# Performance work log

Measured on AMD Instinct MI355X. Metric: run time of the kernel, lower is better.

## Reference

```python
import jax, jax.numpy as jnp
import numpy as np

B, D, N_CLASSES = 8192, 128, 512
MARGIN, GAMMA = 0.25, 256.0
NEG_INF = -1e9  # effectively -inf; logits are O(gamma*2) ~ 512 in magnitude


def setup_inputs() -> dict:
    key = jax.random.key(0)
    k1, k2 = jax.random.split(key)
    feat = jax.random.normal(k1, (B, D), dtype=jnp.float32)
    label = jax.random.randint(k2, (B,), 0, N_CLASSES, dtype=jnp.int64)
    return {"feat": feat, "label": label}


def reference(feat, label):
    m, gamma = MARGIN, GAMMA
    O_p, O_n = 1.0 + m, -m
    delta_p, delta_n = 1.0 - m, m

    # L2-normalize rows (eps clamp as in F.normalize)
    norm = jnp.maximum(jnp.linalg.norm(feat, axis=1, keepdims=True), 1e-12)
    f = feat / norm
    sim = f @ f.T  # [B, B]

    same = label[:, None] == label[None, :]
    eye = jnp.eye(sim.shape[0], dtype=bool)
    pos_mask = same & ~eye
    neg_mask = ~same

    sim_d = jax.lax.stop_gradient(sim)  # .detach() in torch
    alpha_p = jax.nn.relu(O_p - sim_d)
    alpha_n = jax.nn.relu(sim_d - O_n)

    logit_p = -gamma * alpha_p * (sim - delta_p)
    logit_n = gamma * alpha_n * (sim - delta_n)

    # Per-row masked logsumexp over positives / negatives
    lse_p = jax.nn.logsumexp(jnp.where(pos_mask, logit_p, NEG_INF), axis=1)
    lse_n = jax.nn.logsumexp(jnp.where(neg_mask, logit_n, NEG_INF), axis=1)

    # Rows with no positives or no negatives are skipped in the original loop
    valid = pos_mask.any(axis=1) & neg_mask.any(axis=1)
    loss_i = jax.nn.softplus(lse_n + lse_p)
    n_valid = jnp.maximum(valid.sum(), 1)
    return jnp.sum(jnp.where(valid, loss_i, 0.0)) / n_valid
```

## Files before the change

kernel.cpp:

```cpp
#include <hip/hip_runtime.h>
#include <hip/hip_bf16.h>

typedef short bf16x8 __attribute__((ext_vector_type(8)));
typedef float f32x4 __attribute__((ext_vector_type(4)));

#define B_ROWS 8192
#define DIM 128
#define NCLS 512
#define MMAX 64
#define NSLICE 64
#define NPAIR 2080

#define G2 369.32993f
#define G2D16B 87.083121f
#define LN2F 0.69314718056f

__global__ __launch_bounds__(256) void prep_k(const float* __restrict__ feat,
                                              unsigned int* __restrict__ fbp,
                                              int* __restrict__ ctrl) {
    const int T = blockIdx.x;
    const int t = threadIdx.x;
    if (T == 0 && t < 4) ctrl[t] = 0;
    const int rr = t >> 4, q = t & 15;
    const int row = T * 16 + rr;
    const float4* f4 = (const float4*)(feat + row * DIM + q * 8);
    const float4 v0 = f4[0], v1 = f4[1];
    float ss = v0.x * v0.x + v0.y * v0.y + v0.z * v0.z + v0.w * v0.w
             + v1.x * v1.x + v1.y * v1.y + v1.z * v1.z + v1.w * v1.w;
    #pragma unroll
    for (int d = 1; d < 16; d <<= 1) ss += __shfl_xor(ss, d);
    const float inv = 1.0f / fmaxf(sqrtf(ss), 1e-12f);
    const float e[8] = {v0.x, v0.y, v0.z, v0.w, v1.x, v1.y, v1.z, v1.w};
    unsigned int w[4];
    #pragma unroll
    for (int j = 0; j < 4; ++j) {
        __hip_bfloat16 lo = __float2bfloat16(e[2 * j] * inv);
        __hip_bfloat16 hi = __float2bfloat16(e[2 * j + 1] * inv);
        w[j] = (unsigned int)*(unsigned short*)&lo |
               ((unsigned int)*(unsigned short*)&hi << 16);
    }
    const int g = (T * 4 + (q >> 2)) * 256 + (q & 3) * 64 + rr * 4;
    *(uint4*)(fbp + g) = make_uint4(w[0], w[1], w[2], w[3]);
}

#define ELEM(sv) __builtin_amdgcn_exp2f(fminf(fmaf(fmaxf((sv), -0.25f) * fmaxf((sv), -0.25f), G2, -G2D16B), 56.f))

__global__ __launch_bounds__(256, 4) void mega_k(const unsigned short* __restrict__ fb_,
                                                 const int* __restrict__ label,
                                                 float* __restrict__ PR,
                                                 float* __restrict__ lse2_p,
                                                 float* __restrict__ lse2_same) {
    __shared__ float colS[4][128];
    __shared__ unsigned int F[MMAX][MMAX + 1];
    __shared__ int rlw[4][MMAX];
    __shared__ int rl[MMAX];
    __shared__ int cntw[4];

    const int bid = blockIdx.x;
    const int tid = threadIdx.x;
    const int wv = tid >> 6, ln = tid & 63;

    if (bid < NPAIR) {
        int I = (int)((129.0f - sqrtf(16641.0f - 8.0f * (float)bid)) * 0.5f);
        while (I * 64 - I * (I - 1) / 2 > bid) --I;
        while ((I + 1) * 64 - (I + 1) * I / 2 <= bid) ++I;
        const int J = I + (bid - (I * 64 - I * (I - 1) / 2));
        const bool offd = (I != J);

        const int lc = ln & 15, lg = ln >> 4;
        const int wv2 = wv * 2;
        const bf16x8* pk = (const bf16x8*)fb_;

        const int Ta0 = I * 8 + wv2;
        bf16x8 a0[4], a1[4];
        #pragma unroll
        for (int k = 0; k < 4; ++k) {
            a0[k] = pk[(Ta0 * 4 + k) * 64 + ln];
            a1[k] = pk[((Ta0 + 1) * 4 + k) * 64 + ln];
        }

        float Sr0 = 0.f, Sr1 = 0.f;
        bf16x8 bA[4], bB[4];
        const bf16x8* pB = pk + J * 2048 + ln;

        #define LOADB(dst, base) { \
            _Pragma("unroll") \
            for (int k = 0; k < 4; ++k) dst[k] = (base)[k * 64]; }

        #define STEP(bR, t) { \
            f32x4 acc0 = {0.f, 0.f, 0.f, 0.f}, acc1 = acc0; \
            _Pragma("unroll") \
            for (int k = 0; k < 4; ++k) { \
                acc0 = __builtin_amdgcn_mfma_f32_16x16x32_bf16(bR[k], a0[k], acc0, 0, 0, 0); \
                acc1 = __builtin_amdgcn_mfma_f32_16x16x32_bf16(bR[k], a1[k], acc1, 0, 0, 0); \
            } \
            float e00 = ELEM(acc0[0]), e01 = ELEM(acc0[1]); \
            float e02 = ELEM(acc0[2]), e03 = ELEM(acc0[3]); \
            float e10 = ELEM(acc1[0]), e11 = ELEM(acc1[1]); \
            float e12 = ELEM(acc1[2]), e13 = ELEM(acc1[3]); \
            if (!offd && (t) == wv2) { \
                const int base = lg * 4; \
                e00 = (base + 0 == lc) ? 0.f : e00; \
                e01 = (base + 1 == lc) ? 0.f : e01; \
                e02 = (base + 2 == lc) ? 0.f : e02; \
                e03 = (base + 3 == lc) ? 0.f : e03; \
            } \
            if (!offd && (t) == wv2 + 1) { \
                const int base = lg * 4; \
                e10 = (base + 0 == lc) ? 0.f : e10; \
                e11 = (base + 1 == lc) ? 0.f : e11; \
                e12 = (base + 2 == lc) ? 0.f : e12; \
                e13 = (base + 3 == lc) ? 0.f : e13; \
            } \
            Sr0 += (e00 + e01) + (e02 + e03); \
            Sr1 += (e10 + e11) + (e12 + e13); \
            if (offd) { \
                float c0 = e00 + e10, c1 = e01 + e11; \
                float c2 = e02 + e12, c3 = e03 + e13; \
                _Pragma("unroll") \
                for (int d = 1; d < 16; d <<= 1) { \
                    c0 += __shfl_xor(c0, d); c1 += __shfl_xor(c1, d); \
                    c2 += __shfl_xor(c2, d); c3 += __shfl_xor(c3, d); \
                } \
                if (lc == 0) \
                    *(float4*)&colS[wv][(t) * 16 + lg * 4] = make_float4(c0, c1, c2, c3); \
            } }

        LOADB(bA, pB);
        #pragma unroll 1
        for (int t = 0; t < 8; t += 2) {
            LOADB(bB, pB + 256);
            STEP(bA, t);
            if (t + 2 < 8) LOADB(bA, pB + 512);
            STEP(bB, t + 1);
            pB += 512;
        }
        #undef LOADB
        #undef STEP

        #pragma unroll
        for (int d = 16; d < 64; d <<= 1) {
            Sr0 += __shfl_xor(Sr0, d);
            Sr1 += __shfl_xor(Sr1, d);
        }
        if (lg == 0) {
            const int r = I * 128 + wv * 32 + lc;
            PR[J * B_ROWS + r]      = Sr0;
            PR[J * B_ROWS + r + 16] = Sr1;
        }

        if (offd) {
            __syncthreads();
            if (tid < 128) {
                const float tot = colS[0][tid] + colS[1][tid] +
                                  colS[2][tid] + colS[3][tid];
                PR[I * B_ROWS + J * 128 + tid] = tot;
            }
        }
        return;
    }

    const int c = bid - NPAIR;
    {
        int cnt = 0;
        #pragma unroll 1
        for (int it = 0; it < 8; ++it) {
            const int4 L = ((const int4*)label)[wv * 512 + it * 64 + ln];
            const int lv[4] = {L.x, L.y, L.z, L.w};
            #pragma unroll
            for (int j = 0; j < 4; ++j) {
                const bool hit = (lv[j] == c);
                const unsigned long long mask = __ballot(hit);
                const int below = __popcll(mask & ((1ull << ln) - 1ull));
                const int slot = cnt + below;
                if (hit && slot < MMAX) rlw[wv][slot] = wv * 2048 + it * 256 + ln * 4 + j;
                cnt += __popcll(mask);
            }
        }
        if (ln == 0) cntw[wv] = cnt;
    }
    __syncthreads();
    const int c0 = cntw[0], c1 = cntw[1], c2 = cntw[2], c3 = cntw[3];
    const int total = c0 + c1 + c2 + c3;
    const int m = total < MMAX ? total : MMAX;
    if (m == 0) return;
    const bool row_valid = (total >= 2) && (total < B_ROWS);
    {
        const int offs = (wv > 0 ? c0 : 0) + (wv > 1 ? c1 : 0) + (wv > 2 ? c2 : 0);
        const int mycnt = cntw[wv] < MMAX ? cntw[wv] : MMAX;
        if (ln < mycnt) {
            const int slot = offs + ln;
            if (slot < m) rl[slot] = rlw[wv][ln];
        }
    }
    __syncthreads();

    const unsigned int* fbp = (const unsigned int*)fb_;
    for (int i = wv; i < m; i += 4) {
        const int r = rl[i];
        const int g = ((r >> 4) * 4 + (ln >> 4)) * 256 + ((ln >> 2) & 3) * 64 +
                      (r & 15) * 4 + (ln & 3);
        F[i][ln] = fbp[g];
    }
    __syncthreads();

    for (int i = wv; i < m; i += 4) {
        float s = 0.f;
        if (ln < m) {
            #pragma unroll 8
            for (int k = 0; k < 64; ++k) {
                const unsigned int wi = F[i][k], wj = F[ln][k];
                const float li = __uint_as_float(wi << 16);
                const float hi = __uint_as_float(wi & 0xffff0000u);
                const float lj = __uint_as_float(wj << 16);
                const float hj = __uint_as_float(wj & 0xffff0000u);
                s = fmaf(li, lj, s);
                s = fmaf(hi, hj, s);
            }
        }
        const bool act = (ln < m) && (ln != i);
        const float up = 1.25f - s;
        const float lp = act ? G2 * fmaxf(up, 0.f) * (up - 0.5f) : -1e30f;
        const float un = s + 0.25f;
        const float lnn = act ? G2 * fmaxf(un, 0.f) * (un - 0.5f) : -1e30f;
        float Mp = lp, Mn = lnn;
        #pragma unroll
        for (int d = 1; d < 64; d <<= 1) {
            Mp = fmaxf(Mp, __shfl_xor(Mp, d));
            Mn = fmaxf(Mn, __shfl_xor(Mn, d));
        }
        float Sp = act ? __builtin_amdgcn_exp2f(lp - Mp) : 0.f;
        float Sn = act ? __builtin_amdgcn_exp2f(lnn - Mn) : 0.f;
        #pragma unroll
        for (int d = 1; d < 64; d <<= 1) { Sp += __shfl_xor(Sp, d); Sn += __shfl_xor(Sn, d); }
        if (ln == 0) {
            const int row = rl[i];
            lse2_p[row]    = row_valid ? (Mp + __builtin_amdgcn_logf(Sp)) : -1e30f;
            lse2_same[row] = row_valid ? (Mn + __builtin_amdgcn_logf(Sn)) : -1e30f;
        }
    }
}

__global__ __launch_bounds__(256) void finalize_k(const float* __restrict__ PR,
                                                  const float* __restrict__ lse2_p,
                                                  const float* __restrict__ lse2_same,
                                                  int* __restrict__ ctrl,
                                                  float* __restrict__ out) {
    const int r = blockIdx.x * 256 + threadIdx.x;
    float local = 0.f; int c = 0;
    const float lp2 = lse2_p[r];
    if (lp2 > -1e29f) {
        float pa = 0.f, pb = 0.f, pc = 0.f, pd = 0.f;
        #pragma unroll
        for (int s = 0; s < NSLICE; s += 4) {
            pa += PR[(s + 0) * B_ROWS + r];
            pb += PR[(s + 1) * B_ROWS + r];
            pc += PR[(s + 2) * B_ROWS + r];
            pd += PR[(s + 3) * B_ROWS + r];
        }
        const float Sa = (pa + pb) + (pc + pd);
        const float lse2_all = __builtin_amdgcn_logf(Sa) + 64.f;
        const float d = lse2_same[r] - lse2_all;
        const float corr = __builtin_amdgcn_logf(fmaxf(1.f - __builtin_amdgcn_exp2f(d), 1e-30f));
        const float z = LN2F * (lp2 + lse2_all + corr);
        local = fmaxf(z, 0.f) + log1pf(expf(-fabsf(z)));
        c = 1;
    }
    #pragma unroll
    for (int d = 1; d < 64; d <<= 1) { local += __shfl_xor(local, d); c += __shfl_xor(c, d); }
    __shared__ float wsum[4];
    __shared__ int wcnt[4];
    const int wv = threadIdx.x >> 6;
    if ((threadIdx.x & 63) == 0) { wsum[wv] = local; wcnt[wv] = c; }
    __syncthreads();
    if (threadIdx.x == 0) {
        const float ts = wsum[0] + wsum[1] + wsum[2] + wsum[3];
        const int tc = wcnt[0] + wcnt[1] + wcnt[2] + wcnt[3];
        atomicAdd((float*)&ctrl[1], ts);
        atomicAdd(&ctrl[2], tc);
        __threadfence();
        const int ticket = atomicAdd(&ctrl[0], 1);
        if (ticket == (int)gridDim.x - 1) {
            const float gs = atomicAdd((float*)&ctrl[1], 0.0f);
            const int gc = atomicAdd(&ctrl[2], 0);
            out[0] = gs / (float)(gc > 1 ? gc : 1);
        }
    }
}

extern "C" void kernel_launch(void* const* d_in, const int* in_sizes, int n_in,
                              void* d_out, int out_size, void* d_ws, size_t ws_size,
                              hipStream_t stream) {
    const float* feat = (const float*)d_in[0];
    const int* label = (const int*)d_in[1];
    float* out = (float*)d_out;
    char* ws = (char*)d_ws;

    unsigned int* fbp = (unsigned int*)(ws);
    float* PR         = (float*)(ws + (2u << 20));
    float* lse2_p     = (float*)(ws + (4u << 20));
    float* lse2_same  = (float*)(ws + (4u << 20) + 32768);
    int*   ctrl       = (int*)  (ws + (4u << 20) + 65536);

    prep_k<<<NCLS, 256, 0, stream>>>(feat, fbp, ctrl);
    mega_k<<<NPAIR + NCLS, 256, 0, stream>>>((const unsigned short*)fbp, label,
                                             PR, lse2_p, lse2_same);
    finalize_k<<<B_ROWS / 256, 256, 0, stream>>>(PR, lse2_p, lse2_same, ctrl, out);
}
```

Before: 99.71 us.

## Move per-class positive LSE blocks from mega kernel into prep kernel

The per-class block that computes the positive and same-class log-sum-exp moves out of the MFMA pair kernel and into the prep kernel. There it runs alongside the normalization blocks and reads raw fp32 features, normalizing each row itself instead of loading the bf16 packed copy. The aim is to keep the long-tail class blocks from sharing the grid with the tiled MFMA pair blocks, and to shorten the mega kernel. The trade-off is a prep kernel that mixes heterogeneous work, larger shared memory use, and fp32 dot products that cost more per element.

```diff
diff --git a/kernel.cpp b/kernel.cpp
--- a/kernel.cpp
+++ b/kernel.cpp
@@ -16,151 +16,46 @@
 #define LN2F 0.69314718056f
 
 __global__ __launch_bounds__(256) void prep_k(const float* __restrict__ feat,
+                                              const int* __restrict__ label,
                                               unsigned int* __restrict__ fbp,
+                                              float* __restrict__ lse2_p,
+                                              float* __restrict__ lse2_same,
                                               int* __restrict__ ctrl) {
-    const int T = blockIdx.x;
-    const int t = threadIdx.x;
-    if (T == 0 && t < 4) ctrl[t] = 0;
-    const int rr = t >> 4, q = t & 15;
-    const int row = T * 16 + rr;
-    const float4* f4 = (const float4*)(feat + row * DIM + q * 8);
-    const float4 v0 = f4[0], v1 = f4[1];
-    float ss = v0.x * v0.x + v0.y * v0.y + v0.z * v0.z + v0.w * v0.w
-             + v1.x * v1.x + v1.y * v1.y + v1.z * v1.z + v1.w * v1.w;
-    #pragma unroll
-    for (int d = 1; d < 16; d <<= 1) ss += __shfl_xor(ss, d);
-    const float inv = 1.0f / fmaxf(sqrtf(ss), 1e-12f);
-    const float e[8] = {v0.x, v0.y, v0.z, v0.w, v1.x, v1.y, v1.z, v1.w};
-    unsigned int w[4];
-    #pragma unroll
-    for (int j = 0; j < 4; ++j) {
-        __hip_bfloat16 lo = __float2bfloat16(e[2 * j] * inv);
-        __hip_bfloat16 hi = __float2bfloat16(e[2 * j + 1] * inv);
-        w[j] = (unsigned int)*(unsigned short*)&lo |
-               ((unsigned int)*(unsigned short*)&hi << 16);
-    }
-    const int g = (T * 4 + (q >> 2)) * 256 + (q & 3) * 64 + rr * 4;
-    *(uint4*)(fbp + g) = make_uint4(w[0], w[1], w[2], w[3]);
-}
-
-#define ELEM(sv) __builtin_amdgcn_exp2f(fminf(fmaf(fmaxf((sv), -0.25f) * fmaxf((sv), -0.25f), G2, -G2D16B), 56.f))
-
-__global__ __launch_bounds__(256, 4) void mega_k(const unsigned short* __restrict__ fb_,
-                                                 const int* __restrict__ label,
-                                                 float* __restrict__ PR,
-                                                 float* __restrict__ lse2_p,
-                                                 float* __restrict__ lse2_same) {
-    __shared__ float colS[4][128];
-    __shared__ unsigned int F[MMAX][MMAX + 1];
+    const int bid = blockIdx.x;
+    const int tid = threadIdx.x;
+
+    if (bid < 512) {
+        if (bid == 0 && tid < 4) ctrl[tid] = 0;
+        const int T = bid;
+        const int rr = tid >> 4, q = tid & 15;
+        const int row = T * 16 + rr;
+        const float4* f4 = (const float4*)(feat + row * DIM + q * 8);
+        const float4 v0 = f4[0], v1 = f4[1];
+        float ss = v0.x * v0.x + v0.y * v0.y + v0.z * v0.z + v0.w * v0.w
+                 + v1.x * v1.x + v1.y * v1.y + v1.z * v1.z + v1.w * v1.w;
+        #pragma unroll
+        for (int d = 1; d < 16; d <<= 1) ss += __shfl_xor(ss, d);
+        const float inv = 1.0f / fmaxf(sqrtf(ss), 1e-12f);
+        const float e[8] = {v0.x, v0.y, v0.z, v0.w, v1.x, v1.y, v1.z, v1.w};
+        unsigned int w[4];
+        #pragma unroll
+        for (int j = 0; j < 4; ++j) {
+            __hip_bfloat16 lo = __float2bfloat16(e[2 * j] * inv);
+            __hip_bfloat16 hi = __float2bfloat16(e[2 * j + 1] * inv);
+            w[j] = (unsigned int)*(unsigned short*)&lo |
+                   ((unsigned int)*(unsigned short*)&hi << 16);
+        }
+        const int g = (T * 4 + (q >> 2)) * 256 + (q & 3) * 64 + rr * 4;
+        *(uint4*)(fbp + g) = make_uint4(w[0], w[1], w[2], w[3]);
+        return;
+    }
+
+    const int c = bid - 512;
+    const int wv = tid >> 6, ln = tid & 63;
+    __shared__ float F[MMAX][DIM + 1];
     __shared__ int rlw[4][MMAX];
     __shared__ int rl[MMAX];
     __shared__ int cntw[4];
-
-    const int bid = blockIdx.x;
-    const int tid = threadIdx.x;
-    const int wv = tid >> 6, ln = tid & 63;
-
-    if (bid < NPAIR) {
-        int I = (int)((129.0f - sqrtf(16641.0f - 8.0f * (float)bid)) * 0.5f);
-        while (I * 64 - I * (I - 1) / 2 > bid) --I;
-        while ((I + 1) * 64 - (I + 1) * I / 2 <= bid) ++I;
-        const int J = I + (bid - (I * 64 - I * (I - 1) / 2));
-        const bool offd = (I != J);
-
-        const int lc = ln & 15, lg = ln >> 4;
-        const int wv2 = wv * 2;
-        const bf16x8* pk = (const bf16x8*)fb_;
-
-        const int Ta0 = I * 8 + wv2;
-        bf16x8 a0[4], a1[4];
-        #pragma unroll
-        for (int k = 0; k < 4; ++k) {
-            a0[k] = pk[(Ta0 * 4 + k) * 64 + ln];
-            a1[k] = pk[((Ta0 + 1) * 4 + k) * 64 + ln];
-        }
-
-        float Sr0 = 0.f, Sr1 = 0.f;
-        bf16x8 bA[4], bB[4];
-        const bf16x8* pB = pk + J * 2048 + ln;
-
-        #define LOADB(dst, base) { \
-            _Pragma("unroll") \
-            for (int k = 0; k < 4; ++k) dst[k] = (base)[k * 64]; }
-
-        #define STEP(bR, t) { \
-            f32x4 acc0 = {0.f, 0.f, 0.f, 0.f}, acc1 = acc0; \
-            _Pragma("unroll") \
-            for (int k = 0; k < 4; ++k) { \
-                acc0 = __builtin_amdgcn_mfma_f32_16x16x32_bf16(bR[k], a0[k], acc0, 0, 0, 0); \
-                acc1 = __builtin_amdgcn_mfma_f32_16x16x32_bf16(bR[k], a1[k], acc1, 0, 0, 0); \
-            } \
-            float e00 = ELEM(acc0[0]), e01 = ELEM(acc0[1]); \
-            float e02 = ELEM(acc0[2]), e03 = ELEM(acc0[3]); \
-            float e10 = ELEM(acc1[0]), e11 = ELEM(acc1[1]); \
-            float e12 = ELEM(acc1[2]), e13 = ELEM(acc1[3]); \
-            if (!offd && (t) == wv2) { \
-                const int base = lg * 4; \
-                e00 = (base + 0 == lc) ? 0.f : e00; \
-                e01 = (base + 1 == lc) ? 0.f : e01; \
-                e02 = (base + 2 == lc) ? 0.f : e02; \
-                e03 = (base + 3 == lc) ? 0.f : e03; \
-            } \
-            if (!offd && (t) == wv2 + 1) { \
-                const int base = lg * 4; \
-                e10 = (base + 0 == lc) ? 0.f : e10; \
-                e11 = (base + 1 == lc) ? 0.f : e11; \
-                e12 = (base + 2 == lc) ? 0.f : e12; \
-                e13 = (base + 3 == lc) ? 0.f : e13; \
-            } \
-            Sr0 += (e00 + e01) + (e02 + e03); \
-            Sr1 += (e10 + e11) + (e12 + e13); \
-            if (offd) { \
-                float c0 = e00 + e10, c1 = e01 + e11; \
-                float c2 = e02 + e12, c3 = e03 + e13; \
-                _Pragma("unroll") \
-                for (int d = 1; d < 16; d <<= 1) { \
-                    c0 += __shfl_xor(c0, d); c1 += __shfl_xor(c1, d); \
-                    c2 += __shfl_xor(c2, d); c3 += __shfl_xor(c3, d); \
-                } \
-                if (lc == 0) \
-                    *(float4*)&colS[wv][(t) * 16 + lg * 4] = make_float4(c0, c1, c2, c3); \
-            } }
-
-        LOADB(bA, pB);
-        #pragma unroll 1
-        for (int t = 0; t < 8; t += 2) {
-            LOADB(bB, pB + 256);
-            STEP(bA, t);
-            if (t + 2 < 8) LOADB(bA, pB + 512);
-            STEP(bB, t + 1);
-            pB += 512;
-        }
-        #undef LOADB
-        #undef STEP
-
-        #pragma unroll
-        for (int d = 16; d < 64; d <<= 1) {
-            Sr0 += __shfl_xor(Sr0, d);
-            Sr1 += __shfl_xor(Sr1, d);
-        }
-        if (lg == 0) {
-            const int r = I * 128 + wv * 32 + lc;
-            PR[J * B_ROWS + r]      = Sr0;
-            PR[J * B_ROWS + r + 16] = Sr1;
-        }
-
-        if (offd) {
-            __syncthreads();
-            if (tid < 128) {
-                const float tot = colS[0][tid] + colS[1][tid] +
-                                  colS[2][tid] + colS[3][tid];
-                PR[I * B_ROWS + J * 128 + tid] = tot;
-            }
-        }
-        return;
-    }
-
-    const int c = bid - NPAIR;
     {
         int cnt = 0;
         #pragma unroll 1
@@ -195,12 +90,15 @@
     }
     __syncthreads();
 
-    const unsigned int* fbp = (const unsigned int*)fb_;
     for (int i = wv; i < m; i += 4) {
         const int r = rl[i];
-        const int g = ((r >> 4) * 4 + (ln >> 4)) * 256 + ((ln >> 2) & 3) * 64 +
-                      (r & 15) * 4 + (ln & 3);
-        F[i][ln] = fbp[g];
+        const float2 v = ((const float2*)feat)[r * 64 + ln];
+        float ss = v.x * v.x + v.y * v.y;
+        #pragma unroll
+        for (int d = 1; d < 64; d <<= 1) ss += __shfl_xor(ss, d);
+        const float inv = 1.0f / fmaxf(sqrtf(ss), 1e-12f);
+        F[i][2 * ln] = v.x * inv;
+        F[i][2 * ln + 1] = v.y * inv;
     }
     __syncthreads();
 
@@ -208,15 +106,7 @@
         float s = 0.f;
         if (ln < m) {
             #pragma unroll 8
-            for (int k = 0; k < 64; ++k) {
-                const unsigned int wi = F[i][k], wj = F[ln][k];
-                const float li = __uint_as_float(wi << 16);
-                const float hi = __uint_as_float(wi & 0xffff0000u);
-                const float lj = __uint_as_float(wj << 16);
-                const float hj = __uint_as_float(wj & 0xffff0000u);
-                s = fmaf(li, lj, s);
-                s = fmaf(hi, hj, s);
-            }
+            for (int k = 0; k < DIM; ++k) s = fmaf(F[i][k], F[ln][k], s);
         }
         const bool act = (ln < m) && (ln != i);
         const float up = 1.25f - s;
@@ -237,6 +127,113 @@
             const int row = rl[i];
             lse2_p[row]    = row_valid ? (Mp + __builtin_amdgcn_logf(Sp)) : -1e30f;
             lse2_same[row] = row_valid ? (Mn + __builtin_amdgcn_logf(Sn)) : -1e30f;
+        }
+    }
+}
+
+#define ELEM(sv) __builtin_amdgcn_exp2f(fminf(fmaf(fmaxf((sv), -0.25f) * fmaxf((sv), -0.25f), G2, -G2D16B), 56.f))
+
+__global__ __launch_bounds__(256, 4) void mega_k(const unsigned short* __restrict__ fb_,
+                                                 float* __restrict__ PR) {
+    __shared__ float colS[4][128];
+    const int bid = blockIdx.x;
+    const int tid = threadIdx.x;
+    const int wv = tid >> 6, ln = tid & 63;
+
+    int I = (int)((129.0f - sqrtf(16641.0f - 8.0f * (float)bid)) * 0.5f);
+    while (I * 64 - I * (I - 1) / 2 > bid) --I;
+    while ((I + 1) * 64 - (I + 1) * I / 2 <= bid) ++I;
+    const int J = I + (bid - (I * 64 - I * (I - 1) / 2));
+    const bool offd = (I != J);
+
+    const int lc = ln & 15, lg = ln >> 4;
+    const int wv2 = wv * 2;
+    const bf16x8* pk = (const bf16x8*)fb_;
+
+    const int Ta0 = I * 8 + wv2;
+    bf16x8 a0[4], a1[4];
+    #pragma unroll
+    for (int k = 0; k < 4; ++k) {
+        a0[k] = pk[(Ta0 * 4 + k) * 64 + ln];
+        a1[k] = pk[((Ta0 + 1) * 4 + k) * 64 + ln];
+    }
+
+    float Sr0 = 0.f, Sr1 = 0.f;
+    bf16x8 bA[4], bB[4];
+    const bf16x8* pB = pk + J * 2048 + ln;
+
+    #define LOADB(dst, base) { \
+        _Pragma("unroll") \
+        for (int k = 0; k < 4; ++k) dst[k] = (base)[k * 64]; }
+
+    #define STEP(bR, t) { \
+        f32x4 acc0 = {0.f, 0.f, 0.f, 0.f}, acc1 = acc0; \
+        _Pragma("unroll") \
+        for (int k = 0; k < 4; ++k) { \
+            acc0 = __builtin_amdgcn_mfma_f32_16x16x32_bf16(bR[k], a0[k], acc0, 0, 0, 0); \
+            acc1 = __builtin_amdgcn_mfma_f32_16x16x32_bf16(bR[k], a1[k], acc1, 0, 0, 0); \
+        } \
+        float e00 = ELEM(acc0[0]), e01 = ELEM(acc0[1]); \
+        float e02 = ELEM(acc0[2]), e03 = ELEM(acc0[3]); \
+        float e10 = ELEM(acc1[0]), e11 = ELEM(acc1[1]); \
+        float e12 = ELEM(acc1[2]), e13 = ELEM(acc1[3]); \
+        if (!offd && (t) == wv2) { \
+            const int base = lg * 4; \
+            e00 = (base + 0 == lc) ? 0.f : e00; \
+            e01 = (base + 1 == lc) ? 0.f : e01; \
+            e02 = (base + 2 == lc) ? 0.f : e02; \
+            e03 = (base + 3 == lc) ? 0.f : e03; \
+        } \
+        if (!offd && (t) == wv2 + 1) { \
+            const int base = lg * 4; \
+            e10 = (base + 0 == lc) ? 0.f : e10; \
+            e11 = (base + 1 == lc) ? 0.f : e11; \
+            e12 = (base + 2 == lc) ? 0.f : e12; \
+            e13 = (base + 3 == lc) ? 0.f : e13; \
+        } \
+        Sr0 += (e00 + e01) + (e02 + e03); \
+        Sr1 += (e10 + e11) + (e12 + e13); \
+        if (offd) { \
+            float c0 = e00 + e10, c1 = e01 + e11; \
+            float c2 = e02 + e12, c3 = e03 + e13; \
+            _Pragma("unroll") \
+            for (int d = 1; d < 16; d <<= 1) { \
+                c0 += __shfl_xor(c0, d); c1 += __shfl_xor(c1, d); \
+                c2 += __shfl_xor(c2, d); c3 += __shfl_xor(c3, d); \
+            } \
+            if (lc == 0) \
+                *(float4*)&colS[wv][(t) * 16 + lg * 4] = make_float4(c0, c1, c2, c3); \
+        } }
+
+    LOADB(bA, pB);
+    #pragma unroll 1
+    for (int t = 0; t < 8; t += 2) {
+        LOADB(bB, pB + 256);
+        STEP(bA, t);
+        if (t + 2 < 8) LOADB(bA, pB + 512);
+        STEP(bB, t + 1);
+        pB += 512;
+    }
+    #undef LOADB
+    #undef STEP
+
+    #pragma unroll
+    for (int d = 16; d < 64; d <<= 1) {
+        Sr0 += __shfl_xor(Sr0, d);
+        Sr1 += __shfl_xor(Sr1, d);
+    }
+    if (lg == 0) {
+        const int r = I * 128 + wv * 32 + lc;
+        PR[J * B_ROWS + r]      = Sr0;
+        PR[J * B_ROWS + r + 16] = Sr1;
+    }
+
+    if (offd) {
+        __syncthreads();
+        if (tid < 128) {
+            const float tot = colS[0][tid] + colS[1][tid] +
+                              colS[2][tid] + colS[3][tid];
+            PR[I * B_ROWS + J * 128 + tid] = tot;
         }
     }
 }
@@ -302,8 +299,7 @@
     float* lse2_same  = (float*)(ws + (4u << 20) + 32768);
     int*   ctrl       = (int*)  (ws + (4u << 20) + 65536);
 
-    prep_k<<<NCLS, 256, 0, stream>>>(feat, fbp, ctrl);
-    mega_k<<<NPAIR + NCLS, 256, 0, stream>>>((const unsigned short*)fbp, label,
-                                             PR, lse2_p, lse2_same);
+    prep_k<<<1024, 256, 0, stream>>>(feat, label, fbp, lse2_p, lse2_same, ctrl);
+    mega_k<<<NPAIR, 256, 0, stream>>>((const unsigned short*)fbp, PR);
     finalize_k<<<B_ROWS / 256, 256, 0, stream>>>(PR, lse2_p, lse2_same, ctrl, out);
 }
```

Measured after the change: 109.6 us. 1.1x slower.
